# Optimization experiments

Hardware: AMD Instinct MI355X
Metric: run time of the kernel (lower is better)

Reference implementation:

```python
import jax, jax.numpy as jnp
import numpy as np

B, I, O, C, U = 32, 2048, 32, 16, 32  # batch, in_channels(caps), out_capsules, in_capsules(dim), unit_size
NUM_ITERS = 3


def setup_inputs() -> dict:
    key = jax.random.key(0)
    k1, k2 = jax.random.split(key)
    x = jax.random.normal(k1, (B, I, C), dtype=jnp.float32)
    w = jax.random.normal(k2, (I, O, C, U), dtype=jnp.float32)
    return {"x": x, "w": w}


def _squash(v):
    # faithful to original: vec * |vec| / (1 + |vec|^2), norm over last (unit) dim
    n = jnp.linalg.norm(v, axis=-1, keepdims=True)
    return v * n / (1.0 + n * n)


def reference(x, w):
    # u_hat[b,i,o,u] = sum_c x[b,i,c] * w[i,o,c,u]   (the original's x @ w with singleton dims dropped)
    u_hat = jnp.einsum('bic,iocu->biou', x, w)  # [B,I,O,U]
    b_log = jnp.zeros((I, O, 1), dtype=x.dtype)
    v = None
    for _ in range(NUM_ITERS):
        # original computes softmax over dim=2 of [I,O,1] (a singleton dim) -> all ones; kept faithful
        c = jax.nn.softmax(b_log, axis=2)[..., 0]  # [I,O]
        s = jnp.einsum('io,biou->bou', c, u_hat)   # sum over input capsules
        v = _squash(s)                              # [B,O,U]
        # agreement: per-(b,i,o) dot(u_hat, v), then mean over batch (original's update.mean(dim=0))
        agree = jnp.einsum('biou,bou->io', u_hat, v) / B
        b_log = b_log + agree[..., None]
    return v[:, :, None, :]  # matches original v.squeeze(1) -> [B, O, 1, U]
```

## Files before the change

### kernel.cpp

```cpp
#include <hip/hip_runtime.h>
#include <math.h>

#define B_   32
#define I_   2048
#define O_   32
#define C_   16
#define U_   32
#define NCOL (O_ * U_)

#define TI   8
#define OSPL 2
#define OH_  (O_ / OSPL)
#define NIH  (I_ / TI)
#define NBLK (NIH * OSPL)
#define SLICE (B_ * OH_ * U_)
#define XS   36

typedef float f32x4 __attribute__((ext_vector_type(4)));


__global__ __launch_bounds__(512, 4) void caps_partial(const float* __restrict__ x,
                                                       const float* __restrict__ w,
                                                       float* __restrict__ ws) {
    __shared__ float xs[TI * C_ * XS];
    const int tid = threadIdx.x;
    const int ih  = blockIdx.x & (NIH - 1);
    const int oh  = blockIdx.x >> 8;
    const int i0  = ih * TI;
    const int o0  = oh * OH_;

    for (int k = tid; k < B_ * TI * C_; k += 512) {
        int b   = k >> 7;
        int rem = k & 127;
        xs[rem * XS + b] = x[(size_t)b * (I_ * C_) + (size_t)i0 * C_ + rem];
    }
    __syncthreads();

    const int bh = tid >> 7;
    const int ct = tid & 127;
    const int oo = ct >> 3;
    const int u4 = (ct & 7) << 2;
    const float* wp = w + (size_t)i0 * (O_ * C_ * U_) + (size_t)(o0 + oo) * (C_ * U_) + u4;

    float4 acc[8];
#pragma unroll
    for (int b = 0; b < 8; ++b) acc[b] = make_float4(0.f, 0.f, 0.f, 0.f);

    for (int il = 0; il < TI; ++il) {
        const float* wpi = wp + (size_t)il * (O_ * C_ * U_);
        const float* xr  = &xs[(il * C_) * XS + bh * 8];
#pragma unroll
        for (int cc = 0; cc < C_; cc += 8) {
            f32x4 wv[8];
#pragma unroll
            for (int j = 0; j < 8; ++j)
                wv[j] = __builtin_nontemporal_load(
                    (const f32x4*)(wpi + (cc + j) * U_));
#pragma unroll
            for (int j = 0; j < 8; ++j) {
                const float* xc = xr + (cc + j) * XS;
                float4 xa = *(const float4*)(xc);
                float4 xb = *(const float4*)(xc + 4);
                acc[0].x = fmaf(xa.x, wv[j].x, acc[0].x);
                acc[0].y = fmaf(xa.x, wv[j].y, acc[0].y);
                acc[0].z = fmaf(xa.x, wv[j].z, acc[0].z);
                acc[0].w = fmaf(xa.x, wv[j].w, acc[0].w);
                acc[1].x = fmaf(xa.y, wv[j].x, acc[1].x);
                acc[1].y = fmaf(xa.y, wv[j].y, acc[1].y);
                acc[1].z = fmaf(xa.y, wv[j].z, acc[1].z);
                acc[1].w = fmaf(xa.y, wv[j].w, acc[1].w);
                acc[2].x = fmaf(xa.z, wv[j].x, acc[2].x);
                acc[2].y = fmaf(xa.z, wv[j].y, acc[2].y);
                acc[2].z = fmaf(xa.z, wv[j].z, acc[2].z);
                acc[2].w = fmaf(xa.z, wv[j].w, acc[2].w);
                acc[3].x = fmaf(xa.w, wv[j].x, acc[3].x);
                acc[3].y = fmaf(xa.w, wv[j].y, acc[3].y);
                acc[3].z = fmaf(xa.w, wv[j].z, acc[3].z);
                acc[3].w = fmaf(xa.w, wv[j].w, acc[3].w);
                acc[4].x = fmaf(xb.x, wv[j].x, acc[4].x);
                acc[4].y = fmaf(xb.x, wv[j].y, acc[4].y);
                acc[4].z = fmaf(xb.x, wv[j].z, acc[4].z);
                acc[4].w = fmaf(xb.x, wv[j].w, acc[4].w);
                acc[5].x = fmaf(xb.y, wv[j].x, acc[5].x);
                acc[5].y = fmaf(xb.y, wv[j].y, acc[5].y);
                acc[5].z = fmaf(xb.y, wv[j].z, acc[5].z);
                acc[5].w = fmaf(xb.y, wv[j].w, acc[5].w);
                acc[6].x = fmaf(xb.z, wv[j].x, acc[6].x);
                acc[6].y = fmaf(xb.z, wv[j].y, acc[6].y);
                acc[6].z = fmaf(xb.z, wv[j].z, acc[6].z);
                acc[6].w = fmaf(xb.z, wv[j].w, acc[6].w);
                acc[7].x = fmaf(xb.w, wv[j].x, acc[7].x);
                acc[7].y = fmaf(xb.w, wv[j].y, acc[7].y);
                acc[7].z = fmaf(xb.w, wv[j].z, acc[7].z);
                acc[7].w = fmaf(xb.w, wv[j].w, acc[7].w);
            }
        }
    }

    float* op = ws + (size_t)blockIdx.x * SLICE + (size_t)(bh * 8) * (OH_ * U_)
                + oo * U_ + u4;
#pragma unroll
    for (int bl = 0; bl < 8; ++bl)
        *(float4*)(op + (size_t)bl * (OH_ * U_)) = acc[bl];
}

__global__ __launch_bounds__(256) void caps_reduce_squash(const float* __restrict__ ws,
                                                          float* __restrict__ out) {
    __shared__ float sh[128];
    const int tl = threadIdx.x & 127;
    const int ph = threadIdx.x >> 7;
    const int e  = blockIdx.x * 128 + tl;
    const int b  = e >> 10;
    const int o  = (e >> 5) & 31;
    const int u  = e & 31;
    const int oh = o >> 4;
    const int oo = o & 15;
    const float* p = ws + ((size_t)oh * NIH + (size_t)ph * (NIH / 2)) * SLICE
                     + (size_t)b * (OH_ * U_) + oo * U_ + u;
    float s = 0.f;
#pragma unroll 16
    for (int i = 0; i < NIH / 2; ++i)
        s += p[(size_t)i * SLICE];
    if (ph) sh[tl] = s;
    __syncthreads();
    if (ph == 0) {
        s += sh[tl];
        float ss = s * s;
        ss += __shfl_xor(ss, 1);
        ss += __shfl_xor(ss, 2);
        ss += __shfl_xor(ss, 4);
        ss += __shfl_xor(ss, 8);
        ss += __shfl_xor(ss, 16);
        float n = sqrtf(ss);
        out[e] = s * n / (1.0f + ss);
    }
}

#define FTI 4
__global__ __launch_bounds__(256, 2) void caps_main_atomic(const float* __restrict__ x,
                                                           const float* __restrict__ w,
                                                           float* __restrict__ out) {
    __shared__ float xs[FTI * C_ * 33];
    const int tid = threadIdx.x;
    const int i0 = blockIdx.x * FTI;
    for (int k = tid; k < B_ * FTI * C_; k += 256) {
        int b = k >> 6, rem = k & 63;
        xs[rem * 33 + b] = x[(size_t)b * (I_ * C_) + (size_t)i0 * C_ + rem];
    }
    __syncthreads();
    const int o = tid >> 3, u4 = (tid & 7) << 2;
    const float* wp = w + (size_t)i0 * (O_ * C_ * U_) + o * (C_ * U_) + u4;
    float4 acc[B_];
#pragma unroll
    for (int b = 0; b < B_; ++b) acc[b] = make_float4(0.f, 0.f, 0.f, 0.f);
    for (int il = 0; il < FTI; ++il) {
        const float* wpi = wp + (size_t)il * (O_ * C_ * U_);
        const float* xr = &xs[il * C_ * 33];
#pragma unroll
        for (int c = 0; c < C_; ++c) {
            float4 wv = *(const float4*)(wpi + c * U_);
            const float* xc = xr + c * 33;
#pragma unroll
            for (int b = 0; b < B_; ++b) {
                float xb = xc[b];
                acc[b].x = fmaf(xb, wv.x, acc[b].x);
                acc[b].y = fmaf(xb, wv.y, acc[b].y);
                acc[b].z = fmaf(xb, wv.z, acc[b].z);
                acc[b].w = fmaf(xb, wv.w, acc[b].w);
            }
        }
    }
    float* op = out + o * U_ + u4;
#pragma unroll
    for (int b = 0; b < B_; ++b) {
        float* p = op + (size_t)b * NCOL;
        atomicAdd(p + 0, acc[b].x);
        atomicAdd(p + 1, acc[b].y);
        atomicAdd(p + 2, acc[b].z);
        atomicAdd(p + 3, acc[b].w);
    }
}

__global__ void caps_squash_inplace(float* __restrict__ out) {
    int t = blockIdx.x * 256 + threadIdx.x;
    float s = out[t];
    float ss = s * s;
    ss += __shfl_xor(ss, 1);
    ss += __shfl_xor(ss, 2);
    ss += __shfl_xor(ss, 4);
    ss += __shfl_xor(ss, 8);
    ss += __shfl_xor(ss, 16);
    float n = sqrtf(ss);
    out[t] = s * n / (1.0f + ss);
}

extern "C" void kernel_launch(void* const* d_in, const int* in_sizes, int n_in,
                              void* d_out, int out_size, void* d_ws, size_t ws_size,
                              hipStream_t stream) {
    const float* x = (const float*)d_in[0];
    const float* w = (const float*)d_in[1];
    float* out = (float*)d_out;

    const size_t need = (size_t)NBLK * SLICE * sizeof(float);
    if (ws_size >= need) {
        float* ws = (float*)d_ws;
        caps_partial<<<NBLK, 512, 0, stream>>>(x, w, ws);
        caps_reduce_squash<<<(B_ * NCOL) / 128, 256, 0, stream>>>(ws, out);
    } else {
        hipMemsetAsync(out, 0, (size_t)(B_ * NCOL) * sizeof(float), stream);
        caps_main_atomic<<<I_ / FTI, 256, 0, stream>>>(x, w, out);
        caps_squash_inplace<<<(B_ * NCOL) / 256, 256, 0, stream>>>(out);
    }
}
```

Measured before the change: 213.6 us.

## Retile partial kernel to 16 inputs by 8 outputs with 4 batches per thread

The partial-sum kernel now processes 16 input capsules per block, split four ways over output capsules, so each block covers 8 outputs. Each thread holds 4 batch accumulators instead of 8, and the w loads switch from nontemporal to normal loads. The intent is to halve the number of partial slices the reduction kernel reads and to lower register pressure. In exchange, each w value is reused across only 4 batches per thread and there is more shared-memory x traffic per FMA.

```diff
diff --git a/kernel.cpp b/kernel.cpp
--- a/kernel.cpp
+++ b/kernel.cpp
@@ -8,12 +8,12 @@
 #define U_   32
 #define NCOL (O_ * U_)
 
-#define TI   8
-#define OSPL 2
-#define OH_  (O_ / OSPL)
+#define TI   16
+#define OSPL 4
+#define OB_  (O_ / OSPL)
 #define NIH  (I_ / TI)
 #define NBLK (NIH * OSPL)
-#define SLICE (B_ * OH_ * U_)
+#define SLICE (B_ * OB_ * U_)
 #define XS   36
 
 typedef float f32x4 __attribute__((ext_vector_type(4)));
@@ -25,83 +25,65 @@
     __shared__ float xs[TI * C_ * XS];
     const int tid = threadIdx.x;
     const int ih  = blockIdx.x & (NIH - 1);
-    const int oh  = blockIdx.x >> 8;
+    const int oq  = blockIdx.x >> 7;
     const int i0  = ih * TI;
-    const int o0  = oh * OH_;
+    const int o0  = oq * OB_;
 
     for (int k = tid; k < B_ * TI * C_; k += 512) {
-        int b   = k >> 7;
-        int rem = k & 127;
+        int b   = k >> 8;
+        int rem = k & 255;
         xs[rem * XS + b] = x[(size_t)b * (I_ * C_) + (size_t)i0 * C_ + rem];
     }
     __syncthreads();
 
-    const int bh = tid >> 7;
-    const int ct = tid & 127;
+    const int bq = tid >> 6;
+    const int ct = tid & 63;
     const int oo = ct >> 3;
     const int u4 = (ct & 7) << 2;
-    const float* wp = w + (size_t)i0 * (O_ * C_ * U_) + (size_t)(o0 + oo) * (C_ * U_) + u4;
+    const float* wp = w + (size_t)i0 * (O_ * C_ * U_)
+                    + (size_t)(o0 + oo) * (C_ * U_) + u4;
 
-    float4 acc[8];
+    float4 acc[4];
 #pragma unroll
-    for (int b = 0; b < 8; ++b) acc[b] = make_float4(0.f, 0.f, 0.f, 0.f);
+    for (int m = 0; m < 4; ++m) acc[m] = make_float4(0.f, 0.f, 0.f, 0.f);
 
     for (int il = 0; il < TI; ++il) {
         const float* wpi = wp + (size_t)il * (O_ * C_ * U_);
-        const float* xr  = &xs[(il * C_) * XS + bh * 8];
+        const float* xr  = &xs[(il * C_) * XS + bq * 4];
 #pragma unroll
         for (int cc = 0; cc < C_; cc += 8) {
             f32x4 wv[8];
 #pragma unroll
             for (int j = 0; j < 8; ++j)
-                wv[j] = __builtin_nontemporal_load(
-                    (const f32x4*)(wpi + (cc + j) * U_));
+                wv[j] = *(const f32x4*)(wpi + (cc + j) * U_);
 #pragma unroll
             for (int j = 0; j < 8; ++j) {
-                const float* xc = xr + (cc + j) * XS;
-                float4 xa = *(const float4*)(xc);
-                float4 xb = *(const float4*)(xc + 4);
-                acc[0].x = fmaf(xa.x, wv[j].x, acc[0].x);
-                acc[0].y = fmaf(xa.x, wv[j].y, acc[0].y);
-                acc[0].z = fmaf(xa.x, wv[j].z, acc[0].z);
-                acc[0].w = fmaf(xa.x, wv[j].w, acc[0].w);
-                acc[1].x = fmaf(xa.y, wv[j].x, acc[1].x);
-                acc[1].y = fmaf(xa.y, wv[j].y, acc[1].y);
-                acc[1].z = fmaf(xa.y, wv[j].z, acc[1].z);
-                acc[1].w = fmaf(xa.y, wv[j].w, acc[1].w);
-                acc[2].x = fmaf(xa.z, wv[j].x, acc[2].x);
-                acc[2].y = fmaf(xa.z, wv[j].y, acc[2].y);
-                acc[2].z = fmaf(xa.z, wv[j].z, acc[2].z);
-                acc[2].w = fmaf(xa.z, wv[j].w, acc[2].w);
-                acc[3].x = fmaf(xa.w, wv[j].x, acc[3].x);
-                acc[3].y = fmaf(xa.w, wv[j].y, acc[3].y);
-                acc[3].z = fmaf(xa.w, wv[j].z, acc[3].z);
-                acc[3].w = fmaf(xa.w, wv[j].w, acc[3].w);
-                acc[4].x = fmaf(xb.x, wv[j].x, acc[4].x);
-                acc[4].y = fmaf(xb.x, wv[j].y, acc[4].y);
-                acc[4].z = fmaf(xb.x, wv[j].z, acc[4].z);
-                acc[4].w = fmaf(xb.x, wv[j].w, acc[4].w);
-                acc[5].x = fmaf(xb.y, wv[j].x, acc[5].x);
-                acc[5].y = fmaf(xb.y, wv[j].y, acc[5].y);
-                acc[5].z = fmaf(xb.y, wv[j].z, acc[5].z);
-                acc[5].w = fmaf(xb.y, wv[j].w, acc[5].w);
-                acc[6].x = fmaf(xb.z, wv[j].x, acc[6].x);
-                acc[6].y = fmaf(xb.z, wv[j].y, acc[6].y);
-                acc[6].z = fmaf(xb.z, wv[j].z, acc[6].z);
-                acc[6].w = fmaf(xb.z, wv[j].w, acc[6].w);
-                acc[7].x = fmaf(xb.w, wv[j].x, acc[7].x);
-                acc[7].y = fmaf(xb.w, wv[j].y, acc[7].y);
-                acc[7].z = fmaf(xb.w, wv[j].z, acc[7].z);
-                acc[7].w = fmaf(xb.w, wv[j].w, acc[7].w);
+                float4 xq = *(const float4*)(xr + (cc + j) * XS);
+                acc[0].x = fmaf(xq.x, wv[j].x, acc[0].x);
+                acc[0].y = fmaf(xq.x, wv[j].y, acc[0].y);
+                acc[0].z = fmaf(xq.x, wv[j].z, acc[0].z);
+                acc[0].w = fmaf(xq.x, wv[j].w, acc[0].w);
+                acc[1].x = fmaf(xq.y, wv[j].x, acc[1].x);
+                acc[1].y = fmaf(xq.y, wv[j].y, acc[1].y);
+                acc[1].z = fmaf(xq.y, wv[j].z, acc[1].z);
+                acc[1].w = fmaf(xq.y, wv[j].w, acc[1].w);
+                acc[2].x = fmaf(xq.z, wv[j].x, acc[2].x);
+                acc[2].y = fmaf(xq.z, wv[j].y, acc[2].y);
+                acc[2].z = fmaf(xq.z, wv[j].z, acc[2].z);
+                acc[2].w = fmaf(xq.z, wv[j].w, acc[2].w);
+                acc[3].x = fmaf(xq.w, wv[j].x, acc[3].x);
+                acc[3].y = fmaf(xq.w, wv[j].y, acc[3].y);
+                acc[3].z = fmaf(xq.w, wv[j].z, acc[3].z);
+                acc[3].w = fmaf(xq.w, wv[j].w, acc[3].w);
             }
         }
     }
 
-    float* op = ws + (size_t)blockIdx.x * SLICE + (size_t)(bh * 8) * (OH_ * U_)
+    float* op = ws + (size_t)blockIdx.x * SLICE + (size_t)(bq * 4) * (OB_ * U_)
                 + oo * U_ + u4;
 #pragma unroll
-    for (int bl = 0; bl < 8; ++bl)
-        *(float4*)(op + (size_t)bl * (OH_ * U_)) = acc[bl];
+    for (int m = 0; m < 4; ++m)
+        *(float4*)(op + (size_t)m * (OB_ * U_)) = acc[m];
 }
 
 __global__ __launch_bounds__(256) void caps_reduce_squash(const float* __restrict__ ws,
@@ -113,10 +95,10 @@
     const int b  = e >> 10;
     const int o  = (e >> 5) & 31;
     const int u  = e & 31;
-    const int oh = o >> 4;
-    const int oo = o & 15;
-    const float* p = ws + ((size_t)oh * NIH + (size_t)ph * (NIH / 2)) * SLICE
-                     + (size_t)b * (OH_ * U_) + oo * U_ + u;
+    const int oq = o >> 3;
+    const int oo = o & 7;
+    const float* p = ws + ((size_t)oq * NIH + (size_t)ph * (NIH / 2)) * SLICE
+                     + (size_t)b * (OB_ * U_) + oo * U_ + u;
     float s = 0.f;
 #pragma unroll 16
     for (int i = 0; i < NIH / 2; ++i)
```

Result: slower. 219.6 us (+2.8%).
